# Optimization experiments

Measured on AMD Instinct MI355X. Metric: run time of the kernel, lower is better.

The kernel has to match this reference:

```python
import jax, jax.numpy as jnp
import numpy as np

T, N, F_IN, F_H, E = 16, 10000, 32, 64, 160000


def setup_inputs() -> dict:
    key = jax.random.key(0)
    ks = jax.random.split(key, 6)
    x = jax.random.normal(ks[0], (T, N, F_IN), dtype=jnp.float32)
    edge_index = jax.random.randint(ks[1], (2, E), 0, N, dtype=jnp.int64)
    edge_weight = jax.random.uniform(ks[2], (E,), dtype=jnp.float32)
    missing_mask = jnp.zeros((T, N, F_IN), dtype=jnp.bool_)
    # GCNConv params (glorot-ish init, zero bias as in PyG defaults)
    W1 = jax.random.normal(ks[3], (F_IN, F_H), dtype=jnp.float32) / np.float32(np.sqrt(F_IN))
    b1 = jnp.zeros((F_H,), dtype=jnp.float32)
    W2 = jax.random.normal(ks[4], (F_H, F_IN), dtype=jnp.float32) / np.float32(np.sqrt(F_H))
    b2 = jnp.zeros((F_IN,), dtype=jnp.float32)
    return dict(x=x, edge_index=edge_index, edge_weight=edge_weight,
                missing_mask=missing_mask, W1=W1, b1=b1, W2=W2, b2=b2)


def _gcn_norm(edge_index, edge_weight, num_nodes):
    # add self-loops with weight 1, symmetric normalization D^-1/2 (A+I) D^-1/2
    loop = jnp.arange(num_nodes, dtype=edge_index.dtype)
    src = jnp.concatenate([edge_index[0], loop])
    dst = jnp.concatenate([edge_index[1], loop])
    w = jnp.concatenate([edge_weight, jnp.ones((num_nodes,), edge_weight.dtype)])
    deg = jax.ops.segment_sum(w, dst, num_segments=num_nodes)
    dis = jnp.where(deg > 0, jax.lax.rsqrt(jnp.where(deg > 0, deg, 1.0)), 0.0)
    norm = dis[src] * w * dis[dst]
    return src, dst, norm


def _gcn_conv(x, src, dst, norm, W, b):
    # x: (T, N, Fin) -> (T, N, Fout); linear first, then gather-scale-scatter
    xw = jnp.einsum('tnf,fg->tng', x, W)
    msgs = xw[:, src, :] * norm[None, :, None]          # (T, E+N, Fout)
    out = jnp.zeros((x.shape[0], x.shape[1], W.shape[1]), x.dtype)
    out = out.at[:, dst, :].add(msgs)
    return out + b


def reference(x, edge_index, edge_weight, missing_mask, W1, b1, W2, b2):
    num_nodes = x.shape[1]
    src, dst, norm = _gcn_norm(edge_index, edge_weight, num_nodes)
    h = jax.nn.relu(_gcn_conv(x, src, dst, norm, W1, b1))
    out = _gcn_conv(h, src, dst, norm, W2, b2)
    return (out, 0)
```

## Files before the change

### kernel.cpp

```cpp
#include <hip/hip_runtime.h>
#include <hip/hip_bf16.h>

#define T_DIM   16
#define N_NODES 10000
#define FIN     32
#define FH      64
#define NE      160000
#define GPB     8
#define TB      2
#define NCHUNK  (T_DIM / TB)
#define NF      (N_NODES * FIN)

__global__ void build_deg_kernel(const int* __restrict__ ei,
                                 const float* __restrict__ w,
                                 float* __restrict__ deg,
                                 int* __restrict__ cnt) {
    int e = blockIdx.x * blockDim.x + threadIdx.x;
    if (e < NE) {
        int d = ei[NE + e];
        atomicAdd(&deg[d], w[e]);
        atomicAdd(&cnt[d], 1);
    }
}

__global__ void finish_deg_kernel(const float* __restrict__ deg,
                                  float* __restrict__ dis,
                                  float* __restrict__ selfn) {
    int n = blockIdx.x * blockDim.x + threadIdx.x;
    if (n < N_NODES) {
        float d = deg[n] + 1.0f;
        float r = rsqrtf(d);
        dis[n] = r;
        selfn[n] = r * r;
    }
}

__global__ __launch_bounds__(1024) void scan_kernel(const int* __restrict__ cnt,
                                                    int* __restrict__ rowptr) {
    __shared__ int sm[1024];
    int tid = threadIdx.x;
    int base = tid * 10;
    int v[10];
    int s = 0;
#pragma unroll
    for (int k = 0; k < 10; ++k) {
        int i = base + k;
        v[k] = (i < N_NODES) ? cnt[i] : 0;
        s += v[k];
    }
    sm[tid] = s;
    __syncthreads();
    for (int off = 1; off < 1024; off <<= 1) {
        int t = (tid >= off) ? sm[tid - off] : 0;
        __syncthreads();
        sm[tid] += t;
        __syncthreads();
    }
    int run = (tid > 0) ? sm[tid - 1] : 0;
#pragma unroll
    for (int k = 0; k < 10; ++k) {
        int i = base + k;
        if (i <= N_NODES) rowptr[i] = run;
        run += v[k];
    }
}

__global__ void build_csr_kernel(const int* __restrict__ ei,
                                 const float* __restrict__ w,
                                 const float* __restrict__ dis,
                                 const int* __restrict__ rowptr,
                                 int* __restrict__ cursor,
                                 int2* __restrict__ edges) {
    int e = blockIdx.x * blockDim.x + threadIdx.x;
    if (e < NE) {
        int s = ei[e];
        int d = ei[NE + e];
        int pos = rowptr[d] + atomicAdd(&cursor[d], 1);
        edges[pos] = make_int2(s, __float_as_int(dis[s] * w[e] * dis[d]));
    }
}

__global__ __launch_bounds__(256) void layer1_kernel(
    const float* __restrict__ x,
    const int* __restrict__ rowptr,
    const int2* __restrict__ edges,
    const float* __restrict__ selfn,
    const float* __restrict__ W1,
    const float* __restrict__ b1,
    const float* __restrict__ W2,
    float* __restrict__ g) {
    __shared__ float sW1[FIN * FH];
    __shared__ float sW2[FH * FIN];
    __shared__ float sB1[FH];
    __shared__ float sAcc[GPB][TB][FIN];
    __shared__ float sH[GPB][TB][FH];

    int tid = threadIdx.x;
    for (int i = tid; i < FIN * FH; i += 256) sW1[i] = W1[i];
    for (int i = tid; i < FH * FIN; i += 256) sW2[i] = W2[i];
    if (tid < FH) sB1[tid] = b1[tid];

    int b = blockIdx.x;
    int tc = b & (NCHUNK - 1);
    int nb = b >> 3;
    int grp = tid >> 5;
    int lane = tid & 31;
    int n = nb * GPB + grp;

    const float* x0 = x + (size_t)(tc * TB) * NF;

    float sn = selfn[n];
    float a0 = sn * x0[n * FIN + lane];
    float a1 = sn * x0[NF + n * FIN + lane];

    int e = rowptr[n], e1 = rowptr[n + 1];
    for (; e + 4 <= e1; e += 4) {
        int2 p0 = edges[e], p1 = edges[e + 1], p2 = edges[e + 2], p3 = edges[e + 3];
        int c0 = p0.x * FIN + lane, c1 = p1.x * FIN + lane;
        int c2 = p2.x * FIN + lane, c3 = p3.x * FIN + lane;
        float x00 = x0[c0], x01 = x0[NF + c0];
        float x10 = x0[c1], x11 = x0[NF + c1];
        float x20 = x0[c2], x21 = x0[NF + c2];
        float x30 = x0[c3], x31 = x0[NF + c3];
        float v0 = __int_as_float(p0.y), v1 = __int_as_float(p1.y);
        float v2 = __int_as_float(p2.y), v3 = __int_as_float(p3.y);
        a0 = fmaf(v0, x00, a0); a1 = fmaf(v0, x01, a1);
        a0 = fmaf(v1, x10, a0); a1 = fmaf(v1, x11, a1);
        a0 = fmaf(v2, x20, a0); a1 = fmaf(v2, x21, a1);
        a0 = fmaf(v3, x30, a0); a1 = fmaf(v3, x31, a1);
    }
    for (; e < e1; ++e) {
        int2 p = edges[e];
        float v = __int_as_float(p.y);
        int c = p.x * FIN + lane;
        a0 = fmaf(v, x0[c], a0);
        a1 = fmaf(v, x0[NF + c], a1);
    }
    sAcc[grp][0][lane] = a0;
    sAcc[grp][1][lane] = a1;
    __syncthreads();

    float h0 = sB1[lane], h1 = sB1[lane + 32];
    float h2 = h0, h3 = h1;
#pragma unroll
    for (int f = 0; f < FIN; ++f) {
        float w0 = sW1[f * FH + lane];
        float w1 = sW1[f * FH + lane + 32];
        float af0 = sAcc[grp][0][f];
        float af1 = sAcc[grp][1][f];
        h0 = fmaf(af0, w0, h0); h1 = fmaf(af0, w1, h1);
        h2 = fmaf(af1, w0, h2); h3 = fmaf(af1, w1, h3);
    }
    sH[grp][0][lane] = fmaxf(h0, 0.0f);
    sH[grp][0][lane + 32] = fmaxf(h1, 0.0f);
    sH[grp][1][lane] = fmaxf(h2, 0.0f);
    sH[grp][1][lane + 32] = fmaxf(h3, 0.0f);

    float g0 = 0.0f, g1 = 0.0f;
#pragma unroll
    for (int j = 0; j < FH; ++j) {
        float w = sW2[j * FIN + lane];
        g0 = fmaf(sH[grp][0][j], w, g0);
        g1 = fmaf(sH[grp][1][j], w, g1);
    }
    size_t gb = (size_t)n * (T_DIM * FIN) + (tc * TB) * FIN + lane;
    g[gb] = g0;
    g[gb + FIN] = g1;
}

__global__ __launch_bounds__(256) void layer2_kernel(
    const float* __restrict__ g,
    const int* __restrict__ rowptr,
    const int2* __restrict__ edges,
    const float* __restrict__ selfn,
    const float* __restrict__ b2,
    float* __restrict__ out, int out_size) {
    int b = blockIdx.x;
    int tc = b & (NCHUNK - 1);
    int nb = b >> 3;
    int tid = threadIdx.x;
    int grp = tid >> 5;
    int lane = tid & 31;
    int n = nb * GPB + grp;
    int t0 = tc * TB;

    float sn = selfn[n];
    float bb = b2[lane];
    const float* gn = g + (size_t)n * (T_DIM * FIN) + t0 * FIN + lane;
    float a0 = bb + sn * gn[0];
    float a1 = bb + sn * gn[FIN];

    int e = rowptr[n], e1 = rowptr[n + 1];
    for (; e + 4 <= e1; e += 4) {
        int2 p0 = edges[e], p1 = edges[e + 1], p2 = edges[e + 2], p3 = edges[e + 3];
        const float* g0p = g + (size_t)p0.x * (T_DIM * FIN) + t0 * FIN + lane;
        const float* g1p = g + (size_t)p1.x * (T_DIM * FIN) + t0 * FIN + lane;
        const float* g2p = g + (size_t)p2.x * (T_DIM * FIN) + t0 * FIN + lane;
        const float* g3p = g + (size_t)p3.x * (T_DIM * FIN) + t0 * FIN + lane;
        float x00 = g0p[0], x01 = g0p[FIN];
        float x10 = g1p[0], x11 = g1p[FIN];
        float x20 = g2p[0], x21 = g2p[FIN];
        float x30 = g3p[0], x31 = g3p[FIN];
        float v0 = __int_as_float(p0.y), v1 = __int_as_float(p1.y);
        float v2 = __int_as_float(p2.y), v3 = __int_as_float(p3.y);
        a0 = fmaf(v0, x00, a0); a1 = fmaf(v0, x01, a1);
        a0 = fmaf(v1, x10, a0); a1 = fmaf(v1, x11, a1);
        a0 = fmaf(v2, x20, a0); a1 = fmaf(v2, x21, a1);
        a0 = fmaf(v3, x30, a0); a1 = fmaf(v3, x31, a1);
    }
    for (; e < e1; ++e) {
        int2 p = edges[e];
        float v = __int_as_float(p.y);
        const float* gp = g + (size_t)p.x * (T_DIM * FIN) + t0 * FIN + lane;
        a0 = fmaf(v, gp[0], a0);
        a1 = fmaf(v, gp[FIN], a1);
    }

    out[(size_t)t0 * NF + n * FIN + lane] = a0;
    out[(size_t)(t0 + 1) * NF + n * FIN + lane] = a1;

    if (b == 0 && tid == 0) {
        for (int i = T_DIM * NF; i < out_size; ++i) out[i] = 0.0f;
    }
}

extern "C" void kernel_launch(void* const* d_in, const int* in_sizes, int n_in,
                              void* d_out, int out_size, void* d_ws, size_t ws_size,
                              hipStream_t stream) {
    const float* x  = (const float*)d_in[0];
    const int*   ei = (const int*)d_in[1];
    const float* w  = (const float*)d_in[2];
    const float* W1 = (const float*)d_in[4];
    const float* b1 = (const float*)d_in[5];
    const float* W2 = (const float*)d_in[6];
    const float* b2 = (const float*)d_in[7];
    float* out = (float*)d_out;

    char* p = (char*)d_ws;
    float* g      = (float*)p; p += sizeof(float) * (size_t)T_DIM * NF;
    float* deg    = (float*)p; p += sizeof(float) * N_NODES;
    int*   cnt    = (int*)p;   p += sizeof(int) * N_NODES;
    int*   cursor = (int*)p;   p += sizeof(int) * N_NODES;
    float* dis    = (float*)p; p += sizeof(float) * N_NODES;
    float* selfn  = (float*)p; p += sizeof(float) * N_NODES;
    int*   rowptr = (int*)p;   p += sizeof(int) * (N_NODES + 1);
    int2*  edges  = (int2*)p;  p += sizeof(int2) * NE;

    hipMemsetAsync(deg, 0, sizeof(float) * N_NODES * 3, stream);

    build_deg_kernel<<<(NE + 255) / 256, 256, 0, stream>>>(ei, w, deg, cnt);
    finish_deg_kernel<<<(N_NODES + 255) / 256, 256, 0, stream>>>(deg, dis, selfn);
    scan_kernel<<<1, 1024, 0, stream>>>(cnt, rowptr);
    build_csr_kernel<<<(NE + 255) / 256, 256, 0, stream>>>(ei, w, dis, rowptr,
                                                           cursor, edges);
    layer1_kernel<<<(N_NODES / GPB) * NCHUNK, 256, 0, stream>>>(
        x, rowptr, edges, selfn, W1, b1, W2, g);
    layer2_kernel<<<(N_NODES / GPB) * NCHUNK, 256, 0, stream>>>(
        g, rowptr, edges, selfn, b2, out, out_size);
}
```

Measured before the change: 244.0 us.

## Merge setup kernels, drop LDS weight staging, use swizzle broadcasts and packed g layout

Merges the degree-finish and scan kernels into one launch, which also pre-packs W1/W2 into float2 layouts. Layer1 no longer stages weights in shared memory or needs a block barrier; it broadcasts aggregated features across lanes with ds_swizzle and reads weights straight from global/L2. Edge lists are loaded cooperatively 32 at a time and broadcast with shuffles. The intermediate g is stored as interleaved float2 per node and time chunk, so layer2 gathers with one 8-byte load per neighbor. The cost is more global weight reads and swizzle/shuffle instructions, and the ds_swizzle pattern must broadcast correctly within 32-lane groups on a 64-wide wavefront.

```diff
diff --git a/kernel.cpp b/kernel.cpp
--- a/kernel.cpp
+++ b/kernel.cpp
@@ -11,6 +11,20 @@
 #define NCHUNK  (T_DIM / TB)
 #define NF      (N_NODES * FIN)
 
+#define BCAST(v, f) __int_as_float(__builtin_amdgcn_ds_swizzle(__float_as_int(v), ((f) << 5)))
+
+#define DH(f) { float af0 = BCAST(a0, f), af1 = BCAST(a1, f);            \
+                float2 w = W1p[(f) * 32 + lane];                          \
+                h0 = fmaf(af0, w.x, h0); h1 = fmaf(af0, w.y, h1);         \
+                h2 = fmaf(af1, w.x, h2); h3 = fmaf(af1, w.y, h3); }
+#define DG(j) { float2 w = W2p[(j) * 32 + lane];                          \
+                g0 = fmaf(BCAST(r0, j), w.x, g0);                         \
+                g0 = fmaf(BCAST(r1, j), w.y, g0);                         \
+                g1 = fmaf(BCAST(r2, j), w.x, g1);                         \
+                g1 = fmaf(BCAST(r3, j), w.y, g1); }
+#define REP8(M, b) M(b) M(b+1) M(b+2) M(b+3) M(b+4) M(b+5) M(b+6) M(b+7)
+#define REP32(M) REP8(M, 0) REP8(M, 8) REP8(M, 16) REP8(M, 24)
+
 __global__ void build_deg_kernel(const int* __restrict__ ei,
                                  const float* __restrict__ w,
                                  float* __restrict__ deg,
@@ -23,45 +37,54 @@
     }
 }
 
-__global__ void finish_deg_kernel(const float* __restrict__ deg,
-                                  float* __restrict__ dis,
-                                  float* __restrict__ selfn) {
-    int n = blockIdx.x * blockDim.x + threadIdx.x;
-    if (n < N_NODES) {
-        float d = deg[n] + 1.0f;
-        float r = rsqrtf(d);
-        dis[n] = r;
-        selfn[n] = r * r;
-    }
-}
-
-__global__ __launch_bounds__(1024) void scan_kernel(const int* __restrict__ cnt,
-                                                    int* __restrict__ rowptr) {
+__global__ __launch_bounds__(1024) void mid_kernel(
+    const float* __restrict__ deg, float* __restrict__ dis,
+    float* __restrict__ selfn,
+    const int* __restrict__ cnt, int* __restrict__ rowptr,
+    const float* __restrict__ W1, const float* __restrict__ W2,
+    float2* __restrict__ W1p, float2* __restrict__ W2p) {
     __shared__ int sm[1024];
+    int b = blockIdx.x;
     int tid = threadIdx.x;
-    int base = tid * 10;
-    int v[10];
-    int s = 0;
+    if (b < 10) {
+        int n = b * 1024 + tid;
+        if (n < N_NODES) {
+            float d = deg[n] + 1.0f;
+            float r = rsqrtf(d);
+            dis[n] = r;
+            selfn[n] = r * r;
+        }
+    } else if (b == 10) {
+        int base = tid * 10;
+        int v[10];
+        int s = 0;
 #pragma unroll
-    for (int k = 0; k < 10; ++k) {
-        int i = base + k;
-        v[k] = (i < N_NODES) ? cnt[i] : 0;
-        s += v[k];
-    }
-    sm[tid] = s;
-    __syncthreads();
-    for (int off = 1; off < 1024; off <<= 1) {
-        int t = (tid >= off) ? sm[tid - off] : 0;
+        for (int k = 0; k < 10; ++k) {
+            int i = base + k;
+            v[k] = (i < N_NODES) ? cnt[i] : 0;
+            s += v[k];
+        }
+        sm[tid] = s;
         __syncthreads();
-        sm[tid] += t;
-        __syncthreads();
-    }
-    int run = (tid > 0) ? sm[tid - 1] : 0;
+        for (int off = 1; off < 1024; off <<= 1) {
+            int t = (tid >= off) ? sm[tid - off] : 0;
+            __syncthreads();
+            sm[tid] += t;
+            __syncthreads();
+        }
+        int run = (tid > 0) ? sm[tid - 1] : 0;
 #pragma unroll
-    for (int k = 0; k < 10; ++k) {
-        int i = base + k;
-        if (i <= N_NODES) rowptr[i] = run;
-        run += v[k];
+        for (int k = 0; k < 10; ++k) {
+            int i = base + k;
+            if (i <= N_NODES) rowptr[i] = run;
+            run += v[k];
+        }
+    } else if (b == 11) {
+        int f = tid >> 5, l = tid & 31;
+        W1p[tid] = make_float2(W1[f * FH + l], W1[f * FH + 32 + l]);
+    } else {
+        int j = tid >> 5, l = tid & 31;
+        W2p[tid] = make_float2(W2[j * FIN + l], W2[(j + 32) * FIN + l]);
     }
 }
 
@@ -85,24 +108,14 @@
     const int* __restrict__ rowptr,
     const int2* __restrict__ edges,
     const float* __restrict__ selfn,
-    const float* __restrict__ W1,
+    const float2* __restrict__ W1p,
     const float* __restrict__ b1,
-    const float* __restrict__ W2,
-    float* __restrict__ g) {
-    __shared__ float sW1[FIN * FH];
-    __shared__ float sW2[FH * FIN];
-    __shared__ float sB1[FH];
-    __shared__ float sAcc[GPB][TB][FIN];
-    __shared__ float sH[GPB][TB][FH];
-
-    int tid = threadIdx.x;
-    for (int i = tid; i < FIN * FH; i += 256) sW1[i] = W1[i];
-    for (int i = tid; i < FH * FIN; i += 256) sW2[i] = W2[i];
-    if (tid < FH) sB1[tid] = b1[tid];
-
+    const float2* __restrict__ W2p,
+    float2* __restrict__ gp) {
     int b = blockIdx.x;
     int tc = b & (NCHUNK - 1);
     int nb = b >> 3;
+    int tid = threadIdx.x;
     int grp = tid >> 5;
     int lane = tid & 31;
     int n = nb * GPB + grp;
@@ -113,63 +126,35 @@
     float a0 = sn * x0[n * FIN + lane];
     float a1 = sn * x0[NF + n * FIN + lane];
 
-    int e = rowptr[n], e1 = rowptr[n + 1];
-    for (; e + 4 <= e1; e += 4) {
-        int2 p0 = edges[e], p1 = edges[e + 1], p2 = edges[e + 2], p3 = edges[e + 3];
-        int c0 = p0.x * FIN + lane, c1 = p1.x * FIN + lane;
-        int c2 = p2.x * FIN + lane, c3 = p3.x * FIN + lane;
-        float x00 = x0[c0], x01 = x0[NF + c0];
-        float x10 = x0[c1], x11 = x0[NF + c1];
-        float x20 = x0[c2], x21 = x0[NF + c2];
-        float x30 = x0[c3], x31 = x0[NF + c3];
-        float v0 = __int_as_float(p0.y), v1 = __int_as_float(p1.y);
-        float v2 = __int_as_float(p2.y), v3 = __int_as_float(p3.y);
-        a0 = fmaf(v0, x00, a0); a1 = fmaf(v0, x01, a1);
-        a0 = fmaf(v1, x10, a0); a1 = fmaf(v1, x11, a1);
-        a0 = fmaf(v2, x20, a0); a1 = fmaf(v2, x21, a1);
-        a0 = fmaf(v3, x30, a0); a1 = fmaf(v3, x31, a1);
-    }
-    for (; e < e1; ++e) {
-        int2 p = edges[e];
-        float v = __int_as_float(p.y);
-        int c = p.x * FIN + lane;
-        a0 = fmaf(v, x0[c], a0);
-        a1 = fmaf(v, x0[NF + c], a1);
-    }
-    sAcc[grp][0][lane] = a0;
-    sAcc[grp][1][lane] = a1;
-    __syncthreads();
-
-    float h0 = sB1[lane], h1 = sB1[lane + 32];
+    int e0 = rowptr[n], e1 = rowptr[n + 1];
+    for (int base = e0; base < e1; base += 32) {
+        int cnt = min(32, e1 - base);
+        int2 me = make_int2(0, 0);
+        if (lane < cnt) me = edges[base + lane];
+#pragma unroll 4
+        for (int k = 0; k < cnt; ++k) {
+            int c = __shfl(me.x, k, 32);
+            float v = __int_as_float(__shfl(me.y, k, 32));
+            int off = c * FIN + lane;
+            a0 = fmaf(v, x0[off], a0);
+            a1 = fmaf(v, x0[NF + off], a1);
+        }
+    }
+
+    float h0 = b1[lane];
+    float h1 = b1[lane + 32];
     float h2 = h0, h3 = h1;
-#pragma unroll
-    for (int f = 0; f < FIN; ++f) {
-        float w0 = sW1[f * FH + lane];
-        float w1 = sW1[f * FH + lane + 32];
-        float af0 = sAcc[grp][0][f];
-        float af1 = sAcc[grp][1][f];
-        h0 = fmaf(af0, w0, h0); h1 = fmaf(af0, w1, h1);
-        h2 = fmaf(af1, w0, h2); h3 = fmaf(af1, w1, h3);
-    }
-    sH[grp][0][lane] = fmaxf(h0, 0.0f);
-    sH[grp][0][lane + 32] = fmaxf(h1, 0.0f);
-    sH[grp][1][lane] = fmaxf(h2, 0.0f);
-    sH[grp][1][lane + 32] = fmaxf(h3, 0.0f);
-
+    REP32(DH)
+    float r0 = fmaxf(h0, 0.0f), r1 = fmaxf(h1, 0.0f);
+    float r2 = fmaxf(h2, 0.0f), r3 = fmaxf(h3, 0.0f);
     float g0 = 0.0f, g1 = 0.0f;
-#pragma unroll
-    for (int j = 0; j < FH; ++j) {
-        float w = sW2[j * FIN + lane];
-        g0 = fmaf(sH[grp][0][j], w, g0);
-        g1 = fmaf(sH[grp][1][j], w, g1);
-    }
-    size_t gb = (size_t)n * (T_DIM * FIN) + (tc * TB) * FIN + lane;
-    g[gb] = g0;
-    g[gb + FIN] = g1;
+    REP32(DG)
+
+    gp[(n * NCHUNK + tc) * 32 + lane] = make_float2(g0, g1);
 }
 
 __global__ __launch_bounds__(256) void layer2_kernel(
-    const float* __restrict__ g,
+    const float2* __restrict__ gp,
     const int* __restrict__ rowptr,
     const int2* __restrict__ edges,
     const float* __restrict__ selfn,
@@ -182,42 +167,31 @@
     int grp = tid >> 5;
     int lane = tid & 31;
     int n = nb * GPB + grp;
-    int t0 = tc * TB;
 
     float sn = selfn[n];
     float bb = b2[lane];
-    const float* gn = g + (size_t)n * (T_DIM * FIN) + t0 * FIN + lane;
-    float a0 = bb + sn * gn[0];
-    float a1 = bb + sn * gn[FIN];
-
-    int e = rowptr[n], e1 = rowptr[n + 1];
-    for (; e + 4 <= e1; e += 4) {
-        int2 p0 = edges[e], p1 = edges[e + 1], p2 = edges[e + 2], p3 = edges[e + 3];
-        const float* g0p = g + (size_t)p0.x * (T_DIM * FIN) + t0 * FIN + lane;
-        const float* g1p = g + (size_t)p1.x * (T_DIM * FIN) + t0 * FIN + lane;
-        const float* g2p = g + (size_t)p2.x * (T_DIM * FIN) + t0 * FIN + lane;
-        const float* g3p = g + (size_t)p3.x * (T_DIM * FIN) + t0 * FIN + lane;
-        float x00 = g0p[0], x01 = g0p[FIN];
-        float x10 = g1p[0], x11 = g1p[FIN];
-        float x20 = g2p[0], x21 = g2p[FIN];
-        float x30 = g3p[0], x31 = g3p[FIN];
-        float v0 = __int_as_float(p0.y), v1 = __int_as_float(p1.y);
-        float v2 = __int_as_float(p2.y), v3 = __int_as_float(p3.y);
-        a0 = fmaf(v0, x00, a0); a1 = fmaf(v0, x01, a1);
-        a0 = fmaf(v1, x10, a0); a1 = fmaf(v1, x11, a1);
-        a0 = fmaf(v2, x20, a0); a1 = fmaf(v2, x21, a1);
-        a0 = fmaf(v3, x30, a0); a1 = fmaf(v3, x31, a1);
-    }
-    for (; e < e1; ++e) {
-        int2 p = edges[e];
-        float v = __int_as_float(p.y);
-        const float* gp = g + (size_t)p.x * (T_DIM * FIN) + t0 * FIN + lane;
-        a0 = fmaf(v, gp[0], a0);
-        a1 = fmaf(v, gp[FIN], a1);
-    }
-
+    float2 gs = gp[(n * NCHUNK + tc) * 32 + lane];
+    float a0 = fmaf(sn, gs.x, bb);
+    float a1 = fmaf(sn, gs.y, bb);
+
+    int e0 = rowptr[n], e1 = rowptr[n + 1];
+    for (int base = e0; base < e1; base += 32) {
+        int cnt = min(32, e1 - base);
+        int2 me = make_int2(0, 0);
+        if (lane < cnt) me = edges[base + lane];
+#pragma unroll 4
+        for (int k = 0; k < cnt; ++k) {
+            int c = __shfl(me.x, k, 32);
+            float v = __int_as_float(__shfl(me.y, k, 32));
+            float2 gv = gp[(c * NCHUNK + tc) * 32 + lane];
+            a0 = fmaf(v, gv.x, a0);
+            a1 = fmaf(v, gv.y, a1);
+        }
+    }
+
+    int t0 = tc * TB;
     out[(size_t)t0 * NF + n * FIN + lane] = a0;
-    out[(size_t)(t0 + 1) * NF + n * FIN + lane] = a1;
+    out[(size_t)t0 * NF + NF + n * FIN + lane] = a1;
 
     if (b == 0 && tid == 0) {
         for (int i = T_DIM * NF; i < out_size; ++i) out[i] = 0.0f;
@@ -237,7 +211,7 @@
     float* out = (float*)d_out;
 
     char* p = (char*)d_ws;
-    float* g      = (float*)p; p += sizeof(float) * (size_t)T_DIM * NF;
+    float2* gp    = (float2*)p; p += sizeof(float2) * (size_t)N_NODES * NCHUNK * 32;
     float* deg    = (float*)p; p += sizeof(float) * N_NODES;
     int*   cnt    = (int*)p;   p += sizeof(int) * N_NODES;
     int*   cursor = (int*)p;   p += sizeof(int) * N_NODES;
@@ -245,16 +219,18 @@
     float* selfn  = (float*)p; p += sizeof(float) * N_NODES;
     int*   rowptr = (int*)p;   p += sizeof(int) * (N_NODES + 1);
     int2*  edges  = (int2*)p;  p += sizeof(int2) * NE;
+    float2* W1p   = (float2*)p; p += sizeof(float2) * FIN * 32;
+    float2* W2p   = (float2*)p; p += sizeof(float2) * 32 * FIN;
 
     hipMemsetAsync(deg, 0, sizeof(float) * N_NODES * 3, stream);
 
     build_deg_kernel<<<(NE + 255) / 256, 256, 0, stream>>>(ei, w, deg, cnt);
-    finish_deg_kernel<<<(N_NODES + 255) / 256, 256, 0, stream>>>(deg, dis, selfn);
-    scan_kernel<<<1, 1024, 0, stream>>>(cnt, rowptr);
+    mid_kernel<<<13, 1024, 0, stream>>>(deg, dis, selfn, cnt, rowptr,
+                                        W1, W2, W1p, W2p);
     build_csr_kernel<<<(NE + 255) / 256, 256, 0, stream>>>(ei, w, dis, rowptr,
                                                            cursor, edges);
     layer1_kernel<<<(N_NODES / GPB) * NCHUNK, 256, 0, stream>>>(
-        x, rowptr, edges, selfn, W1, b1, W2, g);
+        x, rowptr, edges, selfn, W1p, b1, W2p, gp);
     layer2_kernel<<<(N_NODES / GPB) * NCHUNK, 256, 0, stream>>>(
-        g, rowptr, edges, selfn, b2, out, out_size);
-}
+        gp, rowptr, edges, selfn, b2, out, out_size);
+}
```

Measured after the change: 283.0 us. 1.16x slower.
